# Performance work log

Hardware: AMD Instinct MI355X
Metric: run time of the kernel (lower is better)

Reference implementation:

```python
import jax, jax.numpy as jnp
import numpy as np
from jax import lax


def setup_inputs() -> dict:
    key = jax.random.key(0)
    k1, k2, k3, k4 = jax.random.split(key, 4)
    bs, depth, h, w = 32, 512, 28, 28
    out_c, kh, kw = 512, 3, 3
    x = jax.random.uniform(k1, (bs, depth, h, w), dtype=jnp.float32)
    weight = jax.random.normal(k2, (out_c, depth, kh, kw), dtype=jnp.float32) * 0.02
    bias = jax.random.normal(k3, (out_c,), dtype=jnp.float32) * 0.02
    mask_weight = jax.random.uniform(k4, (depth,), dtype=jnp.float32)
    filt = jnp.ones((depth, 1), dtype=jnp.float32)  # filter==1 -> channel is masked
    return {"x": x, "weight": weight, "bias": bias, "mask_weight": mask_weight,
            "filter": filt, "padding": 1}


def _get_mu(x):
    # x: [bs, depth, h, w]; coordinates are 1-based as in the torch code
    bs, depth, h, w = x.shape
    ix = jnp.arange(1, h + 1, dtype=x.dtype).reshape(1, 1, h, 1)  # row coord
    iy = jnp.arange(1, w + 1, dtype=x.dtype).reshape(1, 1, 1, w)  # col coord
    sumX = jnp.maximum(x.sum((2, 3)), 1e-9)                       # [bs, depth]
    mu_x = jnp.maximum(jnp.round((ix * x).sum((2, 3)) / sumX), 1.0)
    mu_y = jnp.maximum(jnp.round((iy * x).sum((2, 3)) / sumX), 1.0)
    # map integer centroid (1..h) to linspace(-1, 1, h); original uses h for both axes
    lin = jnp.linspace(-1.0, 1.0, h, dtype=x.dtype)
    mu_xg = lin[(mu_x - 1.0).astype(jnp.int32)]                   # [bs, depth]
    mu_yg = lin[(mu_y - 1.0).astype(jnp.int32)]
    return mu_xg, mu_yg


def _get_mask(x, mask_weight, filt):
    bs, depth, h, w = x.shape
    mu_x, mu_y = _get_mu(x)                                        # [bs, depth] each
    posX = jnp.linspace(-1.0, 1.0, h, dtype=x.dtype).reshape(1, 1, h, 1)
    posY = jnp.linspace(-1.0, 1.0, w, dtype=x.dtype).reshape(1, 1, 1, w)
    m = jnp.abs(posX - mu_x[:, :, None, None]) + jnp.abs(posY - mu_y[:, :, None, None])
    m = 1.0 - m * mask_weight.reshape(1, depth, 1, 1)
    m = jnp.maximum(m, -1.0)
    # channels whose filter entry != 1 are unmasked (mask forced to 1)
    m = jnp.where(filt.reshape(1, depth, 1, 1) == 1.0, m, 1.0)
    return m


def reference(x, weight, bias, mask_weight, filter, padding):
    mask = _get_mask(x, mask_weight, filter)
    x_relu = jnp.maximum(x * mask, 0.0)
    out = lax.conv_general_dilated(
        x_relu, weight,
        window_strides=(1, 1),
        padding=[(padding, padding), (padding, padding)],
        dimension_numbers=("NCHW", "OIHW", "NCHW"))
    return out + bias.reshape(1, -1, 1, 1)
```

## Files before the change

### kernel.cpp

```cpp
#include <hip/hip_runtime.h>
#include <stdint.h>

typedef unsigned short u16;
typedef __attribute__((ext_vector_type(8))) short bf16x8;
typedef __attribute__((ext_vector_type(4))) float f32x4;

#define NB 32
#define CH 512
#define HH 28
#define HP 30
#define KTOT 4608
#define BM 128
#define BN 112
#define BK 64
#define ASZ (BM*BK)
#define BSZ (BN*BK)
#define KSTEPS 72

__device__ __forceinline__ u16 f2bf(float f) {
    uint32_t u = __float_as_uint(f);
    uint32_t r = (u + 0x7fffu + ((u >> 16) & 1u)) >> 16;
    return (u16)r;
}

__global__ __launch_bounds__(256) void stats_kernel(
    const float* __restrict__ x, float* __restrict__ muX, float* __restrict__ muY)
{
    int pair = blockIdx.x * 4 + (threadIdx.x >> 6);
    int lane = threadIdx.x & 63;
    const float* xp = x + (size_t)pair * 784;
    float s = 0.f, sx = 0.f, sy = 0.f;
    for (int e = lane; e < 784; e += 64) {
        float v = xp[e];
        int i = e / 28, j = e - i * 28;
        s += v;
        sx += (float)(i + 1) * v;
        sy += (float)(j + 1) * v;
    }
    #pragma unroll
    for (int off = 32; off > 0; off >>= 1) {
        s  += __shfl_down(s, off);
        sx += __shfl_down(sx, off);
        sy += __shfl_down(sy, off);
    }
    if (lane == 0) {
        float S = fmaxf(s, 1e-9f);
        float mx = fmaxf(rintf(sx / S), 1.0f);
        float my = fmaxf(rintf(sy / S), 1.0f);
        int ix = (int)(mx - 1.0f); if (ix > 27) ix = 27;
        int iy = (int)(my - 1.0f); if (iy > 27) iy = 27;
        muX[pair] = -1.0f + (2.0f / 27.0f) * (float)ix;
        muY[pair] = -1.0f + (2.0f / 27.0f) * (float)iy;
    }
}

#define TSTR 520
__global__ __launch_bounds__(256) void mask_relu_transpose(
    const float* __restrict__ x, const float* __restrict__ mw,
    const float* __restrict__ filt, const float* __restrict__ muX,
    const float* __restrict__ muY, u16* __restrict__ xr_pad)
{
    __shared__ u16 tile[28 * TSTR];
    int bid = blockIdx.x;
    int b = bid / 28, i = bid - (bid / 28) * 28;
    int tid = threadIdx.x;
    float px = -1.0f + (2.0f / 27.0f) * (float)i;
    const float* xb = x + (size_t)b * CH * 784 + i * 28;
    const float* muXb = muX + b * CH;
    const float* muYb = muY + b * CH;
    #pragma unroll 8
    for (int k = 0; k < 56; ++k) {
        int e = tid + k * 256;
        int c = e / 28, j = e - c * 28;
        float v = xb[c * 784 + j];
        float py = -1.0f + (2.0f / 27.0f) * (float)j;
        float m = 1.0f - (fabsf(px - muXb[c]) + fabsf(py - muYb[c])) * mw[c];
        m = fmaxf(m, -1.0f);
        if (filt[c] != 1.0f) m = 1.0f;
        tile[j * TSTR + c] = f2bf(fmaxf(v * m, 0.0f));
    }
    __syncthreads();
    u16* outb = xr_pad + (((size_t)b * HP + (i + 1)) * HP + 1) * CH;
    #pragma unroll
    for (int k = 0; k < 7; ++k) {
        int ch = tid + k * 256;
        int j = ch >> 6;
        int c0 = (ch & 63) << 3;
        *reinterpret_cast<uint4*>(outb + (size_t)j * CH + c0) =
            *reinterpret_cast<const uint4*>(&tile[j * TSTR + c0]);
    }
}

__global__ __launch_bounds__(256) void weight_reorder(
    const float* __restrict__ w, u16* __restrict__ w_r)
{
    __shared__ u16 t[KTOT];
    int oc = blockIdx.x;
    const float* wrow = w + (size_t)oc * KTOT;
    int tid = threadIdx.x;
    #pragma unroll
    for (int k = 0; k < 18; ++k) {
        int idx = tid + k * 256;
        int ic = idx / 9, tap = idx - ic * 9;
        t[tap * 512 + ic] = f2bf(wrow[idx]);
    }
    __syncthreads();
    u16* dst = w_r + (size_t)oc * KTOT;
    #pragma unroll
    for (int k = 0; k < 3; ++k) {
        int ch = tid + k * 256;
        if (ch < 576)
            *reinterpret_cast<uint4*>(dst + ch * 8) =
                *reinterpret_cast<const uint4*>(&t[ch * 8]);
    }
}

__global__ __launch_bounds__(256, 2) void conv_gemm(
    const u16* __restrict__ w_r, const u16* __restrict__ xr_pad,
    const float* __restrict__ bias, float* __restrict__ out)
{
    __shared__ __align__(16) u16 smem[2][ASZ + BSZ];
    int p = blockIdx.x;
    int bid = (p & 7) * 112 + (p >> 3);
    int b = bid / 28;
    int rem = bid - b * 28;
    int m0 = (rem / 7) * BM;
    int n0 = (rem - (rem / 7) * 7) * BN;
    int tid = threadIdx.x;
    int lane = tid & 63;
    int wv = tid >> 6;

    uint32_t aoff[4], boff[4], ldsoff[4];
    #pragma unroll
    for (int it = 0; it < 4; ++it) {
        int c = tid * 16 + it * 4096;
        int row = c >> 7;
        int scol = (c & 127) ^ ((row & 7) << 4);
        aoff[it] = (uint32_t)(m0 + row) * KTOT + (scol >> 1);
        ldsoff[it] = c >> 1;
        int n = n0 + (row < BN ? row : 0);
        int oh = n / 28, ow = n - oh * 28;
        boff[it] = (uint32_t)(((b * HP + oh) * HP + ow) * CH) + (scol >> 1);
    }

    auto stage = [&](int buf, int ks) {
        u16* sA = &smem[buf][0];
        u16* sB = &smem[buf][ASZ];
        int koff = ks * 64;
        #pragma unroll
        for (int it = 0; it < 4; ++it) {
            __builtin_amdgcn_global_load_lds(
                (const __attribute__((address_space(1))) uint32_t*)(w_r + aoff[it] + koff),
                (__attribute__((address_space(3))) uint32_t*)(sA + ldsoff[it]),
                16, 0, 0);
        }
        int tap = ks >> 3;
        int kh = tap / 3, kw = tap - kh * 3;
        int xoff = (kh * HP + kw) * CH + (ks & 7) * 64;
        #pragma unroll
        for (int it = 0; it < 4; ++it) {
            if (tid * 16 + it * 4096 < BSZ * 2) {
                __builtin_amdgcn_global_load_lds(
                    (const __attribute__((address_space(1))) uint32_t*)(xr_pad + boff[it] + xoff),
                    (__attribute__((address_space(3))) uint32_t*)(sB + ldsoff[it]),
                    16, 0, 0);
            }
        }
    };

    f32x4 acc[2][7];
    #pragma unroll
    for (int mi = 0; mi < 2; ++mi)
        #pragma unroll
        for (int ni = 0; ni < 7; ++ni)
            acc[mi][ni] = (f32x4){0.f, 0.f, 0.f, 0.f};

    int r15 = lane & 15;
    int rq = lane >> 4;
    int xorv = (r15 & 7) << 4;
    int cb0 = (((rq * 16)      ) ^ xorv) >> 1;
    int cb1 = (((rq * 16) + 64 ) ^ xorv) >> 1;
    int arow = (wv * 32 + r15) * BK;
    int brow = r15 * BK;

    stage(0, 0);
    for (int ks = 0; ks < KSTEPS; ++ks) {
        __syncthreads();
        if (ks + 1 < KSTEPS) stage((ks + 1) & 1, ks + 1);
        const u16* sA = &smem[ks & 1][0];
        const u16* sB = &smem[ks & 1][ASZ];
        #pragma unroll
        for (int kk = 0; kk < 2; ++kk) {
            int cb = kk ? cb1 : cb0;
            bf16x8 a0 = *reinterpret_cast<const bf16x8*>(sA + arow + cb);
            bf16x8 a1 = *reinterpret_cast<const bf16x8*>(sA + arow + 1024 + cb);
            #pragma unroll
            for (int ni = 0; ni < 7; ++ni) {
                bf16x8 bv = *reinterpret_cast<const bf16x8*>(sB + brow + ni * 1024 + cb);
                acc[0][ni] = __builtin_amdgcn_mfma_f32_16x16x32_bf16(a0, bv, acc[0][ni], 0, 0, 0);
                acc[1][ni] = __builtin_amdgcn_mfma_f32_16x16x32_bf16(a1, bv, acc[1][ni], 0, 0, 0);
            }
        }
    }

    float* outb = out + (size_t)b * CH * 784;
    #pragma unroll
    for (int mi = 0; mi < 2; ++mi) {
        #pragma unroll
        for (int ni = 0; ni < 7; ++ni) {
            f32x4 v = acc[mi][ni];
            int row0 = m0 + wv * 32 + mi * 16 + rq * 4;
            int col = n0 + ni * 16 + r15;
            #pragma unroll
            for (int r = 0; r < 4; ++r) {
                int row = row0 + r;
                outb[(size_t)row * 784 + col] = v[r] + bias[row];
            }
        }
    }
}

extern "C" void kernel_launch(void* const* d_in, const int* in_sizes, int n_in,
                              void* d_out, int out_size, void* d_ws, size_t ws_size,
                              hipStream_t stream)
{
    const float* x    = (const float*)d_in[0];
    const float* wgt  = (const float*)d_in[1];
    const float* bias = (const float*)d_in[2];
    const float* mw   = (const float*)d_in[3];
    const float* filt = (const float*)d_in[4];

    const size_t XR_BYTES = (size_t)NB * HP * HP * CH * 2;
    const size_t WR_BYTES = (size_t)CH * KTOT * 2;
    u16* xr_pad = (u16*)d_ws;
    u16* w_r    = (u16*)((char*)d_ws + XR_BYTES);
    float* muX  = (float*)((char*)d_ws + XR_BYTES + WR_BYTES);
    float* muY  = (float*)((char*)d_ws + XR_BYTES + WR_BYTES + 65536);

    hipMemsetAsync(xr_pad, 0, XR_BYTES, stream);
    hipLaunchKernelGGL(stats_kernel, dim3(4096), dim3(256), 0, stream, x, muX, muY);
    hipLaunchKernelGGL(mask_relu_transpose, dim3(NB * 28), dim3(256), 0, stream,
                       x, mw, filt, muX, muY, xr_pad);
    hipLaunchKernelGGL(weight_reorder, dim3(512), dim3(256), 0, stream, wgt, w_r);
    hipLaunchKernelGGL(conv_gemm, dim3(NB * 4 * 7), dim3(256), 0, stream,
                       w_r, xr_pad, bias, (float*)d_out);
}
```

Before: 265.6 us.

## Enlarge conv GEMM tiles to 256x224 with 8 waves spanning batches

The implicit-GEMM conv kernel moves from 128x112 tiles with 4 waves to 256x224 tiles with 8 waves arranged 4x2. The N dimension now runs across batch boundaries, so each wave computes 4x7 MFMA tiles. The aim is to raise arithmetic intensity and cut global and LDS traffic per FLOP. In exchange the grid drops to 224 blocks, which is under one wave of blocks at 2 per CU on 256 CUs, and register pressure from 112 accumulator floats per thread goes up, which may limit occupancy.

```diff
diff --git a/kernel.cpp b/kernel.cpp
--- a/kernel.cpp
+++ b/kernel.cpp
@@ -7,14 +7,14 @@
 
 #define NB 32
 #define CH 512
-#define HH 28
 #define HP 30
 #define KTOT 4608
-#define BM 128
-#define BN 112
+#define BM 256
+#define BN 224
 #define BK 64
-#define ASZ (BM*BK)
-#define BSZ (BN*BK)
+#define ABYTES 32768
+#define BBYTES 28672
+#define BUFU16 30720
 #define KSTEPS 72
 
 __device__ __forceinline__ u16 f2bf(float f) {
@@ -115,107 +115,113 @@
     }
 }
 
-__global__ __launch_bounds__(256, 2) void conv_gemm(
+__global__ __launch_bounds__(512, 2) void conv_gemm(
     const u16* __restrict__ w_r, const u16* __restrict__ xr_pad,
     const float* __restrict__ bias, float* __restrict__ out)
 {
-    __shared__ __align__(16) u16 smem[2][ASZ + BSZ];
+    __shared__ __align__(16) u16 smem[2][BUFU16];
     int p = blockIdx.x;
-    int bid = (p & 7) * 112 + (p >> 3);
-    int b = bid / 28;
-    int rem = bid - b * 28;
-    int m0 = (rem / 7) * BM;
-    int n0 = (rem - (rem / 7) * 7) * BN;
+    int bid = (p & 7) * 28 + (p >> 3);
+    int mt = bid / 112, nt = bid - mt * 112;
+    int m0 = mt * 256;
+    int n0 = nt * 224;
     int tid = threadIdx.x;
     int lane = tid & 63;
-    int wv = tid >> 6;
-
-    uint32_t aoff[4], boff[4], ldsoff[4];
+    int w = tid >> 6;
+    int wm = w >> 1, wn = w & 1;
+
+    uint32_t aoff[4], boff[4], ldsA[4], ldsB[4];
+    bool bmask[4];
     #pragma unroll
     for (int it = 0; it < 4; ++it) {
-        int c = tid * 16 + it * 4096;
+        int c = tid * 16 + it * 8192;
         int row = c >> 7;
         int scol = (c & 127) ^ ((row & 7) << 4);
         aoff[it] = (uint32_t)(m0 + row) * KTOT + (scol >> 1);
-        ldsoff[it] = c >> 1;
-        int n = n0 + (row < BN ? row : 0);
-        int oh = n / 28, ow = n - oh * 28;
-        boff[it] = (uint32_t)(((b * HP + oh) * HP + ow) * CH) + (scol >> 1);
+        ldsA[it] = c >> 1;
+        bmask[it] = (c < BBYTES);
+        int rb = (row < BN) ? row : 0;
+        int n = n0 + rb;
+        int b2 = n / 784, s2 = n - b2 * 784;
+        int oh = s2 / 28, ow = s2 - oh * 28;
+        boff[it] = (uint32_t)(((b2 * HP + oh) * HP + ow) * CH) + (scol >> 1);
+        ldsB[it] = (ABYTES >> 1) + (uint32_t)((c < BBYTES ? c : 0) >> 1);
     }
 
     auto stage = [&](int buf, int ks) {
-        u16* sA = &smem[buf][0];
-        u16* sB = &smem[buf][ASZ];
+        u16* sA = smem[buf];
+        u16* sB = smem[buf] + (ABYTES >> 1);
         int koff = ks * 64;
+        int tap = ks >> 3;
+        int kh = tap / 3, kw = tap - kh * 3;
+        int xoff = (kh * HP + kw) * CH + (ks & 7) * 64;
         #pragma unroll
         for (int it = 0; it < 4; ++it) {
             __builtin_amdgcn_global_load_lds(
                 (const __attribute__((address_space(1))) uint32_t*)(w_r + aoff[it] + koff),
-                (__attribute__((address_space(3))) uint32_t*)(sA + ldsoff[it]),
+                (__attribute__((address_space(3))) uint32_t*)(sA + ldsA[it]),
                 16, 0, 0);
         }
-        int tap = ks >> 3;
-        int kh = tap / 3, kw = tap - kh * 3;
-        int xoff = (kh * HP + kw) * CH + (ks & 7) * 64;
         #pragma unroll
         for (int it = 0; it < 4; ++it) {
-            if (tid * 16 + it * 4096 < BSZ * 2) {
+            if (bmask[it]) {
                 __builtin_amdgcn_global_load_lds(
                     (const __attribute__((address_space(1))) uint32_t*)(xr_pad + boff[it] + xoff),
-                    (__attribute__((address_space(3))) uint32_t*)(sB + ldsoff[it]),
+                    (__attribute__((address_space(3))) uint32_t*)(sB + (ldsB[it] - (ABYTES >> 1))),
                     16, 0, 0);
             }
         }
     };
 
-    f32x4 acc[2][7];
-    #pragma unroll
-    for (int mi = 0; mi < 2; ++mi)
+    f32x4 acc[4][7];
+    #pragma unroll
+    for (int m = 0; m < 4; ++m)
         #pragma unroll
         for (int ni = 0; ni < 7; ++ni)
-            acc[mi][ni] = (f32x4){0.f, 0.f, 0.f, 0.f};
+            acc[m][ni] = (f32x4){0.f, 0.f, 0.f, 0.f};
 
     int r15 = lane & 15;
     int rq = lane >> 4;
     int xorv = (r15 & 7) << 4;
-    int cb0 = (((rq * 16)      ) ^ xorv) >> 1;
-    int cb1 = (((rq * 16) + 64 ) ^ xorv) >> 1;
-    int arow = (wv * 32 + r15) * BK;
-    int brow = r15 * BK;
+    int cb0 = ((rq * 16) ^ xorv) >> 1;
+    int cb1 = ((rq * 16 + 64) ^ xorv) >> 1;
+    int arow = (wm * 64 + r15) * 64;
+    int brow = (ABYTES >> 1) + (wn * 112 + r15) * 64;
 
     stage(0, 0);
     for (int ks = 0; ks < KSTEPS; ++ks) {
         __syncthreads();
         if (ks + 1 < KSTEPS) stage((ks + 1) & 1, ks + 1);
-        const u16* sA = &smem[ks & 1][0];
-        const u16* sB = &smem[ks & 1][ASZ];
+        const u16* sm = smem[ks & 1];
         #pragma unroll
         for (int kk = 0; kk < 2; ++kk) {
             int cb = kk ? cb1 : cb0;
-            bf16x8 a0 = *reinterpret_cast<const bf16x8*>(sA + arow + cb);
-            bf16x8 a1 = *reinterpret_cast<const bf16x8*>(sA + arow + 1024 + cb);
+            bf16x8 a[4];
+            #pragma unroll
+            for (int m = 0; m < 4; ++m)
+                a[m] = *reinterpret_cast<const bf16x8*>(sm + arow + m * 1024 + cb);
             #pragma unroll
             for (int ni = 0; ni < 7; ++ni) {
-                bf16x8 bv = *reinterpret_cast<const bf16x8*>(sB + brow + ni * 1024 + cb);
-                acc[0][ni] = __builtin_amdgcn_mfma_f32_16x16x32_bf16(a0, bv, acc[0][ni], 0, 0, 0);
-                acc[1][ni] = __builtin_amdgcn_mfma_f32_16x16x32_bf16(a1, bv, acc[1][ni], 0, 0, 0);
+                bf16x8 bv = *reinterpret_cast<const bf16x8*>(sm + brow + ni * 1024 + cb);
+                #pragma unroll
+                for (int m = 0; m < 4; ++m)
+                    acc[m][ni] = __builtin_amdgcn_mfma_f32_16x16x32_bf16(a[m], bv, acc[m][ni], 0, 0, 0);
             }
         }
     }
 
-    float* outb = out + (size_t)b * CH * 784;
-    #pragma unroll
-    for (int mi = 0; mi < 2; ++mi) {
+    #pragma unroll
+    for (int m = 0; m < 4; ++m) {
+        int row = m0 + wm * 64 + m * 16 + rq * 4;
         #pragma unroll
         for (int ni = 0; ni < 7; ++ni) {
-            f32x4 v = acc[mi][ni];
-            int row0 = m0 + wv * 32 + mi * 16 + rq * 4;
-            int col = n0 + ni * 16 + r15;
+            int n = n0 + wn * 112 + ni * 16 + r15;
+            int b2 = n / 784, s2 = n - b2 * 784;
+            float* op = out + ((size_t)b2 * CH + row) * 784 + s2;
+            f32x4 v = acc[m][ni];
             #pragma unroll
-            for (int r = 0; r < 4; ++r) {
-                int row = row0 + r;
-                outb[(size_t)row * 784 + col] = v[r] + bias[row];
-            }
+            for (int r = 0; r < 4; ++r)
+                op[(size_t)r * 784] = v[r] + bias[row + r];
         }
     }
 }
@@ -242,6 +248,6 @@
     hipLaunchKernelGGL(mask_relu_transpose, dim3(NB * 28), dim3(256), 0, stream,
                        x, mw, filt, muX, muY, xr_pad);
     hipLaunchKernelGGL(weight_reorder, dim3(512), dim3(256), 0, stream, wgt, w_r);
-    hipLaunchKernelGGL(conv_gemm, dim3(NB * 4 * 7), dim3(256), 0, stream,
+    hipLaunchKernelGGL(conv_gemm, dim3(224), dim3(512), 0, stream,
                        w_r, xr_pad, bias, (float*)d_out);
 }
```

Result: faster. 248.7 us (-6.3%).
